# Optimization experiments

Hardware: AMD Instinct MI355X
Metric: run time of the kernel (lower is better)

The kernel has to match this reference:

```python
import jax, jax.numpy as jnp
import numpy as np


def _ln(x, g, b):
    m = x.mean(-1, keepdims=True)
    v = ((x - m) ** 2).mean(-1, keepdims=True)
    return (x - m) / jnp.sqrt(v + 1e-5) * g + b


def setup_inputs() -> dict:
    B, N, NC, EC = 4, 512, 128, 32
    KN, KE = 10, 5
    OC = 2 * EC  # NodeEdgeCombiner out_channels = 2*edge_channels
    key = jax.random.key(0)
    ks = jax.random.split(key, 16)
    s = lambda k, *sh: jax.random.normal(k, sh, jnp.float32) * 0.05
    return dict(
        node=jax.random.normal(ks[0], (B, N, NC), jnp.float32),
        edge=jax.random.normal(ks[1], (B, N, N, EC), jnp.float32),
        block_id=jnp.sort(jax.random.randint(ks[2], (B, N), 0, 16), axis=-1),
        virtual_mask=jax.random.bernoulli(ks[3], 0.1, (B, N)),
        W_nt=s(ks[4], 2 * EC + NC, NC), b_nt=jnp.zeros((NC,), jnp.float32),
        W_n1=s(ks[5], NC, 2 * OC), b_n1=jnp.zeros((2 * OC,), jnp.float32),
        W_e1=s(ks[6], EC, OC), b_e1=jnp.zeros((OC,), jnp.float32),
        W_f1=s(ks[7], OC, OC), b_f1=jnp.zeros((OC,), jnp.float32),
        W_f2=s(ks[8], OC, OC), b_f2=jnp.zeros((OC,), jnp.float32),
        W_no1=s(ks[9], NC, NC), b_no1=jnp.zeros((NC,), jnp.float32),
        g_no=jnp.ones((NC,), jnp.float32), be_no=jnp.zeros((NC,), jnp.float32),
        W_no2=s(ks[10], NC, KN), b_no2=jnp.zeros((KN,), jnp.float32),
        W_eo1=s(ks[11], OC, EC), b_eo1=jnp.zeros((EC,), jnp.float32),
        g_eo=jnp.ones((EC,), jnp.float32), be_eo=jnp.zeros((EC,), jnp.float32),
        W_eo2=s(ks[12], EC, KE), b_eo2=jnp.zeros((KE,), jnp.float32),
    )


def reference(node, edge, block_id, virtual_mask,
              W_nt, b_nt, W_n1, b_n1, W_e1, b_e1, W_f1, b_f1, W_f2, b_f2,
              W_no1, b_no1, g_no, be_no, W_no2, b_no2,
              W_eo1, b_eo1, g_eo, be_eo, W_eo2, b_eo2):
    silu = jax.nn.silu
    # masks from block ids
    nm = block_id >= 0                                   # B x N node mask
    bi = block_id[:, :, None]
    bj = block_id[:, None, :]
    pv = nm[:, :, None] & nm[:, None, :]
    # causal block mask: i may see j in strictly earlier blocks, or same block
    # unless i is a virtual (next-block placeholder) node
    causal = pv & ((bi > bj) | ((bi == bj) & ~virtual_mask[:, :, None]))
    em = causal | jnp.swapaxes(causal, 1, 2)             # symmetric edge mask
    nodem = node * nm[..., None]
    edgem = edge * em[..., None]
    # edge_to_node: masked mean of causal incoming & outgoing edges -> 2*EC
    c = causal.astype(edge.dtype)
    x_in = jnp.einsum('bijc,bij->bic', edgem, c) / jnp.maximum(c.sum(2), 1.0)[..., None]
    x_out = jnp.einsum('bjic,bji->bic', edgem, c) / jnp.maximum(c.sum(1), 1.0)[..., None]
    # node_transform: Linear + SiLU, then re-mask
    h = silu(jnp.concatenate([x_in, x_out, nodem], -1) @ W_nt + b_nt) * nm[..., None]
    # NodeEdgeCombiner (simple=False)
    e = edgem @ W_e1 + b_e1                              # B x N x N x OC
    n = h @ W_n1 + b_n1                                  # B x N x 2*OC
    n1, n2 = jnp.split(n, 2, axis=-1)
    npair = n1[:, None, :, :] + n2[:, :, None, :]        # outer-sum: n1[j]+n2[i]
    e = silu(npair + e + silu(npair @ W_f1 + b_f1) * silu(e @ W_f2 + b_f2))
    e = e + jnp.swapaxes(e, 1, 2)                        # symmetrize
    e = e * em[..., None]
    # output MLP heads (Linear -> LN -> SiLU -> Linear), masked
    node_logit = (silu(_ln(h @ W_no1 + b_no1, g_no, be_no)) @ W_no2 + b_no2) * nm[..., None]
    edge_logit = (silu(_ln(e @ W_eo1 + b_eo1, g_eo, be_eo)) @ W_eo2 + b_eo2) * em[..., None]
    return node_logit, edge_logit
```

## Files before the change

### kernel.cpp

```cpp
#include <hip/hip_runtime.h>

#define NQ 512
#define NC 128
#define EC 32
#define OC 64

__device__ __forceinline__ float silu_f(float x) {
    return x / (1.0f + __expf(-x));
}

__global__ void decode_mask_kernel(const unsigned char* __restrict__ raw,
                                   int* __restrict__ out, int n) {
    __shared__ int cntA, cntN;
    int t = threadIdx.x;
    if (t == 0) { cntA = 0; cntN = 0; }
    __syncthreads();
    int la = 0, ln = 0;
    for (int idx = t; idx < n; idx += blockDim.x) {
        unsigned char v = raw[idx];
        if (v) { if ((idx & 3) == 0) la++; else ln++; }
    }
    if (la) atomicAdd(&cntA, la);
    if (ln) atomicAdd(&cntN, ln);
    __syncthreads();
    int a = cntA, nn = cntN;
    for (int i = t; i < n; i += blockDim.x) {
        int v;
        if (a > 0 && nn == 0)      v = ((const int*)raw)[i];
        else if (a == 0)           v = (((const float*)raw)[i] != 0.0f);
        else                       v = (raw[i] != 0);
        out[i] = v;
    }
}

__global__ __launch_bounds__(128) void node_kernel(
    const float* __restrict__ node, const float* __restrict__ edge,
    const int* __restrict__ block_id, const int* __restrict__ vmd,
    const float* __restrict__ W_nt, const float* __restrict__ b_nt,
    const float* __restrict__ W_n1, const float* __restrict__ b_n1,
    const float* __restrict__ W_f1, const float* __restrict__ b_f1,
    const float* __restrict__ W_no1, const float* __restrict__ b_no1,
    const float* __restrict__ g_no, const float* __restrict__ be_no,
    const float* __restrict__ W_no2, const float* __restrict__ b_no2,
    float* __restrict__ n_ws, float* __restrict__ q1_ws, float* __restrict__ q2_ws,
    float* __restrict__ out_node) {
    const int bi = blockIdx.x;
    const int b = bi >> 9, i = bi & (NQ - 1);
    const int t = threadIdx.x;

    __shared__ int   sid[NQ];
    __shared__ int   svm[NQ];
    __shared__ float xcat[192];
    __shared__ float rin[4][32];
    __shared__ float rout[4][32];
    __shared__ int   rcin[4], rcout[4];
    __shared__ float hbuf[128];
    __shared__ float red[128];
    __shared__ float nbuf[128];
    __shared__ float zbuf[128];

    for (int k = t; k < NQ; k += 128) {
        sid[k] = block_id[b * NQ + k];
        svm[k] = vmd[b * NQ + k];
    }
    __syncthreads();

    const int  id_i = sid[i];
    const int  vm_i = svm[i];
    const bool nm_i = (id_i >= 0);

    const int c = t & 31, g = t >> 5;
    float accin = 0.f, accout = 0.f;
    int   cntin = 0, cntout = 0;
    const float* erow = edge + ((size_t)(b * NQ + i)) * NQ * EC;
    const float* ecol = edge + ((size_t)b * NQ * NQ + i) * EC;
    for (int j = g; j < NQ; j += 4) {
        int  id_j = sid[j];
        bool nm_j = (id_j >= 0);
        bool pv = nm_i && nm_j;
        bool cin  = pv && ((id_i > id_j) || (id_i == id_j && !vm_i));
        bool cout = pv && ((id_j > id_i) || (id_j == id_i && !svm[j]));
        if (cin)  { accin  += erow[j * EC + c]; cntin++; }
        if (cout) { accout += ecol[(size_t)j * NQ * EC + c]; cntout++; }
    }
    rin[g][c] = accin;
    rout[g][c] = accout;
    if (c == 0) { rcin[g] = cntin; rcout[g] = cntout; }
    __syncthreads();

    if (t < 32) {
        float s = rin[0][t] + rin[1][t] + rin[2][t] + rin[3][t];
        float cnt = (float)(rcin[0] + rcin[1] + rcin[2] + rcin[3]);
        xcat[t] = s / fmaxf(cnt, 1.0f);
    } else if (t < 64) {
        int tc = t - 32;
        float s = rout[0][tc] + rout[1][tc] + rout[2][tc] + rout[3][tc];
        float cnt = (float)(rcout[0] + rcout[1] + rcout[2] + rcout[3]);
        xcat[t] = s / fmaxf(cnt, 1.0f);
    }
    {
        float nv = node[(size_t)(b * NQ + i) * NC + t];
        xcat[64 + t] = nm_i ? nv : 0.0f;
    }
    __syncthreads();

    float acc = b_nt[t];
    #pragma unroll 4
    for (int k = 0; k < 192; ++k) acc += xcat[k] * W_nt[k * NC + t];
    float h = nm_i ? silu_f(acc) : 0.0f;
    hbuf[t] = h;
    __syncthreads();

    float accn = b_n1[t];
    float u = b_no1[t];
    #pragma unroll 4
    for (int k = 0; k < 128; ++k) {
        float hk = hbuf[k];
        accn += hk * W_n1[k * 128 + t];
        u    += hk * W_no1[k * 128 + t];
    }
    n_ws[(size_t)(b * NQ + i) * 128 + t] = accn;

    nbuf[t] = accn;
    red[t] = u;
    __syncthreads();

    {
        int cc = t & 63;
        const float* src = nbuf + ((t < 64) ? 0 : 64);
        float q = (t < 64) ? 0.0f : b_f1[cc];
        #pragma unroll 4
        for (int k = 0; k < 64; ++k) q += src[k] * W_f1[k * 64 + cc];
        float* dst = (t < 64) ? q1_ws : q2_ws;
        dst[(size_t)(b * NQ + i) * 64 + cc] = q;
    }

    for (int s = 64; s > 0; s >>= 1) { if (t < s) red[t] += red[t + s]; __syncthreads(); }
    float m = red[0] * (1.0f / 128.0f);
    __syncthreads();
    float d = u - m;
    red[t] = d * d;
    __syncthreads();
    for (int s = 64; s > 0; s >>= 1) { if (t < s) red[t] += red[t + s]; __syncthreads(); }
    float var = red[0] * (1.0f / 128.0f);
    float z = silu_f(d * rsqrtf(var + 1e-5f) * g_no[t] + be_no[t]);
    zbuf[t] = z;
    __syncthreads();

    if (t < 10) {
        float o = b_no2[t];
        #pragma unroll 4
        for (int k2 = 0; k2 < 128; ++k2) o += zbuf[k2] * W_no2[k2 * 10 + t];
        out_node[(size_t)(b * NQ + i) * 10 + t] = nm_i ? o : 0.0f;
    }
}

__global__ __launch_bounds__(256, 4) void edge_kernel(
    const float* __restrict__ edge, const int* __restrict__ block_id,
    const int* __restrict__ vmd, const float* __restrict__ n_ws,
    const float* __restrict__ q1_ws, const float* __restrict__ q2_ws,
    const float* __restrict__ W_e1, const float* __restrict__ b_e1,
    const float* __restrict__ W_f2, const float* __restrict__ b_f2,
    const float* __restrict__ W_eo1, const float* __restrict__ b_eo1,
    const float* __restrict__ g_eo, const float* __restrict__ be_eo,
    const float* __restrict__ W_eo2, const float* __restrict__ b_eo2,
    float* __restrict__ out_edge) {
    __shared__ float einT[32][64];
    __shared__ float e0T[64][64];
    __shared__ float red2[2][4][64];
    __shared__ float oBuf[4][64][5];

    const int tid = threadIdx.x;
    const int p = tid & 63;
    const int w = __builtin_amdgcn_readfirstlane(tid >> 6);
    const int bid = blockIdx.x;

    int b, ib0, jb0;
    bool tail;
    if (bid < 8192) {
        b = bid >> 11;
        int rem = bid & 2047;
        ib0 = rem >> 2;
        jb0 = ib0 + (rem & 3) * 64;
        tail = false;
    } else {
        int t2 = bid - 8192;
        b = t2 >> 2;
        ib0 = (t2 & 3) * 64;
        jb0 = 0;
        tail = true;
    }
    const int i_p = tail ? (ib0 + p) : ib0;
    const int j_p = tail ? (i_p + 256) : ((jb0 + p) & (NQ - 1));

    const float* nb0 = n_ws  + (size_t)b * NQ * 128;
    const float* q1t = q1_ws + (size_t)b * NQ * 64;
    const float* q2t = q2_ws + (size_t)b * NQ * 64;

    float es[16];
    #pragma unroll
    for (int u = 0; u < 16; ++u) es[u] = 0.0f;

    #pragma unroll 1
    for (int d = 0; d < 2; ++d) {
        {
            const int pr = tid >> 2, u = tid & 3;
            const int i_r = tail ? (ib0 + pr) : ib0;
            const int j_r = tail ? (i_r + 256) : ((jb0 + pr) & (NQ - 1));
            const size_t rowbase = d == 0
                ? (((size_t)(b * NQ) + i_r) * NQ + j_r) * EC
                : (((size_t)(b * NQ) + j_r) * NQ + i_r) * EC;
            const float4* src = (const float4*)(edge + rowbase);
            float4 v0 = src[u];
            float4 v1 = src[u + 4];
            einT[4 * u + 0][pr] = v0.x; einT[4 * u + 1][pr] = v0.y;
            einT[4 * u + 2][pr] = v0.z; einT[4 * u + 3][pr] = v0.w;
            einT[4 * (u + 4) + 0][pr] = v1.x; einT[4 * (u + 4) + 1][pr] = v1.y;
            einT[4 * (u + 4) + 2][pr] = v1.z; einT[4 * (u + 4) + 3][pr] = v1.w;
        }
        __syncthreads();

        float e0c[16];
        #pragma unroll
        for (int u = 0; u < 16; ++u) e0c[u] = b_e1[w * 16 + u];
        #pragma unroll 4
        for (int k = 0; k < EC; ++k) {
            float ek = einT[k][p];
            const float* wr = W_e1 + k * OC + w * 16;
            #pragma unroll
            for (int u = 0; u < 16; ++u) e0c[u] += ek * wr[u];
        }
        #pragma unroll
        for (int u = 0; u < 16; ++u) e0T[w * 16 + u][p] = e0c[u];
        __syncthreads();

        float t2a[16];
        #pragma unroll
        for (int u = 0; u < 16; ++u) t2a[u] = b_f2[w * 16 + u];
        #pragma unroll 4
        for (int k = 0; k < OC; ++k) {
            float e0k = e0T[k][p];
            const float* wr = W_f2 + k * OC + w * 16;
            #pragma unroll
            for (int u = 0; u < 16; ++u) t2a[u] += e0k * wr[u];
        }

        {
            const int ja = d == 0 ? j_p : i_p;
            const int ib = d == 0 ? i_p : j_p;
            const float* pq1 = q1t + (size_t)ja * 64 + w * 16;
            const float* pq2 = q2t + (size_t)ib * 64 + w * 16;
            const float* pn1 = nb0 + (size_t)ja * 128 + w * 16;
            const float* pn2 = nb0 + (size_t)ib * 128 + 64 + w * 16;
            #pragma unroll
            for (int v4 = 0; v4 < 4; ++v4) {
                float4 a1 = ((const float4*)pq1)[v4];
                float4 a2 = ((const float4*)pq2)[v4];
                float4 b1 = ((const float4*)pn1)[v4];
                float4 b2 = ((const float4*)pn2)[v4];
                float q1r[4] = {a1.x, a1.y, a1.z, a1.w};
                float q2r[4] = {a2.x, a2.y, a2.z, a2.w};
                float n1r[4] = {b1.x, b1.y, b1.z, b1.w};
                float n2r[4] = {b2.x, b2.y, b2.z, b2.w};
                #pragma unroll
                for (int r = 0; r < 4; ++r) {
                    int c = v4 * 4 + r;
                    float t1 = silu_f(q1r[r] + q2r[r]);
                    float t2 = silu_f(t2a[c]);
                    es[c] += silu_f(n1r[r] + n2r[r] + e0c[c] + t1 * t2);
                }
            }
        }
        __syncthreads();
    }

    #pragma unroll
    for (int u = 0; u < 16; ++u) e0T[w * 16 + u][p] = es[u];
    __syncthreads();

    const int c0 = w * 8;
    float y[8];
    #pragma unroll
    for (int u = 0; u < 8; ++u) y[u] = b_eo1[c0 + u];
    #pragma unroll 4
    for (int k = 0; k < OC; ++k) {
        float esk = e0T[k][p];
        const float* wr = W_eo1 + k * 32 + c0;
        #pragma unroll
        for (int u = 0; u < 8; ++u) y[u] += esk * wr[u];
    }

    float s1 = 0.f, s2 = 0.f;
    #pragma unroll
    for (int u = 0; u < 8; ++u) { s1 += y[u]; s2 += y[u] * y[u]; }
    red2[0][w][p] = s1;
    red2[1][w][p] = s2;
    __syncthreads();
    float S1 = red2[0][0][p] + red2[0][1][p] + red2[0][2][p] + red2[0][3][p];
    float S2 = red2[1][0][p] + red2[1][1][p] + red2[1][2][p] + red2[1][3][p];
    float mean = S1 * (1.0f / 32.0f);
    float var  = S2 * (1.0f / 32.0f) - mean * mean;
    float rs = rsqrtf(var + 1e-5f);

    float o[5] = {0.f, 0.f, 0.f, 0.f, 0.f};
    #pragma unroll
    for (int u = 0; u < 8; ++u) {
        float z = silu_f((y[u] - mean) * rs * g_eo[c0 + u] + be_eo[c0 + u]);
        const float* wr = W_eo2 + (c0 + u) * 5;
        #pragma unroll
        for (int q = 0; q < 5; ++q) o[q] += z * wr[q];
    }
    #pragma unroll
    for (int q = 0; q < 5; ++q) oBuf[w][p][q] = o[q];
    __syncthreads();

    if (w == 0) {
        const int id_i = block_id[b * NQ + i_p], id_j = block_id[b * NQ + j_p];
        const int vm_i = vmd[b * NQ + i_p],      vm_j = vmd[b * NQ + j_p];
        const bool em = (id_i >= 0) && (id_j >= 0) &&
                        ((id_i != id_j) || (!vm_i) || (!vm_j));
        float* oe1 = out_edge + (((size_t)(b * NQ) + i_p) * NQ + j_p) * 5;
        float* oe2 = out_edge + (((size_t)(b * NQ) + j_p) * NQ + i_p) * 5;
        #pragma unroll
        for (int q = 0; q < 5; ++q) {
            float vq = b_eo2[q] + oBuf[0][p][q] + oBuf[1][p][q]
                                + oBuf[2][p][q] + oBuf[3][p][q];
            vq = em ? vq : 0.0f;
            oe1[q] = vq;
            oe2[q] = vq;
        }
    }
}

extern "C" void kernel_launch(void* const* d_in, const int* in_sizes, int n_in,
                              void* d_out, int out_size, void* d_ws, size_t ws_size,
                              hipStream_t stream) {
    const float* node     = (const float*)d_in[0];
    const float* edge     = (const float*)d_in[1];
    const int*   block_id = (const int*)d_in[2];
    const void*  vm_raw   = d_in[3];
    const float* W_nt  = (const float*)d_in[4];
    const float* b_nt  = (const float*)d_in[5];
    const float* W_n1  = (const float*)d_in[6];
    const float* b_n1  = (const float*)d_in[7];
    const float* W_e1  = (const float*)d_in[8];
    const float* b_e1  = (const float*)d_in[9];
    const float* W_f1  = (const float*)d_in[10];
    const float* b_f1  = (const float*)d_in[11];
    const float* W_f2  = (const float*)d_in[12];
    const float* b_f2  = (const float*)d_in[13];
    const float* W_no1 = (const float*)d_in[14];
    const float* b_no1 = (const float*)d_in[15];
    const float* g_no  = (const float*)d_in[16];
    const float* be_no = (const float*)d_in[17];
    const float* W_no2 = (const float*)d_in[18];
    const float* b_no2 = (const float*)d_in[19];
    const float* W_eo1 = (const float*)d_in[20];
    const float* b_eo1 = (const float*)d_in[21];
    const float* g_eo  = (const float*)d_in[22];
    const float* be_eo = (const float*)d_in[23];
    const float* W_eo2 = (const float*)d_in[24];
    const float* b_eo2 = (const float*)d_in[25];

    char* ws = (char*)d_ws;
    int*   vmd  = (int*)ws;
    float* n_ws = (float*)(ws + 8192);
    float* q1_ws = (float*)(ws + 8192 + (1 << 20));
    float* q2_ws = (float*)(ws + 8192 + (1 << 20) + (512 << 10));
    float* out_node = (float*)d_out;
    float* out_edge = out_node + 4 * 512 * 10;

    decode_mask_kernel<<<1, 256, 0, stream>>>((const unsigned char*)vm_raw, vmd, 4 * 512);
    node_kernel<<<4 * 512, 128, 0, stream>>>(
        node, edge, block_id, vmd,
        W_nt, b_nt, W_n1, b_n1, W_f1, b_f1, W_no1, b_no1, g_no, be_no, W_no2, b_no2,
        n_ws, q1_ws, q2_ws, out_node);
    edge_kernel<<<8192 + 16, 256, 0, stream>>>(
        edge, block_id, vmd, n_ws, q1_ws, q2_ws,
        W_e1, b_e1, W_f2, b_f2,
        W_eo1, b_eo1, g_eo, be_eo, W_eo2, b_eo2, out_edge);
}
```

Before: 598.1 us.

## Split masked edge row/column sums into tiled partial-sum kernel; pad edge LDS

Moves the masked incoming/outgoing edge mean out of the per-node kernel into a separate 64x64 tile kernel. Each tile reads its edge block once, writes per-tile partial sums for both directions, and the node kernel then reduces eight partials per node. This replaces the old strided column gather (stride N*EC), which had poor coalescing. The edge kernel also overlays its LDS buffers with padding (stride 66) and raises the occupancy hint from 4 to 6 waves. The cost is an extra launch and a workspace round trip, and the tile kernel only launches 256 blocks.

```diff
diff --git a/kernel.cpp b/kernel.cpp
--- a/kernel.cpp
+++ b/kernel.cpp
@@ -33,9 +33,78 @@
     }
 }
 
-__global__ __launch_bounds__(128) void node_kernel(
-    const float* __restrict__ node, const float* __restrict__ edge,
-    const int* __restrict__ block_id, const int* __restrict__ vmd,
+__global__ __launch_bounds__(256) void tile_sum_kernel(
+    const float* __restrict__ edge, const int* __restrict__ block_id,
+    const int* __restrict__ vmd,
+    float* __restrict__ xin_part, float* __restrict__ xout_part) {
+    __shared__ float wmask[64][64];
+    __shared__ int idI[64], vmI[64], idJ[64], vmJ[64];
+
+    const int t = threadIdx.x;
+    const int bid = blockIdx.x;
+    const int b = bid >> 6, It = (bid >> 3) & 7, Jt = bid & 7;
+    const int I0 = It * 64, J0 = Jt * 64;
+
+    if (t < 64)       { idI[t] = block_id[b * NQ + I0 + t]; vmI[t] = vmd[b * NQ + I0 + t]; }
+    else if (t < 128) { int u = t - 64; idJ[u] = block_id[b * NQ + J0 + u]; vmJ[u] = vmd[b * NQ + J0 + u]; }
+    __syncthreads();
+
+    for (int idx = t; idx < 4096; idx += 256) {
+        int a = idx >> 6, bb = idx & 63;
+        int ida = idI[a], idb = idJ[bb];
+        bool w = (ida >= 0) && (idb >= 0) &&
+                 ((ida > idb) || (ida == idb && !vmI[a]));
+        wmask[a][bb] = w ? 1.0f : 0.0f;
+    }
+    __syncthreads();
+
+    const float* base = edge + (((size_t)(b * NQ) + I0) * NQ + J0) * EC;
+
+    {
+        const int bb1 = t >> 3, c0 = (t & 7) * 4;
+        float a1x = 0.f, a1y = 0.f, a1z = 0.f, a1w = 0.f;
+        float a2x = 0.f, a2y = 0.f, a2z = 0.f, a2w = 0.f;
+        for (int a = 0; a < 64; ++a) {
+            const float4* row = (const float4*)(base + (size_t)a * NQ * EC);
+            float4 v1 = row[t];
+            float4 v2 = row[t + 256];
+            float w1 = wmask[a][bb1];
+            float w2 = wmask[a][bb1 + 32];
+            a1x += w1 * v1.x; a1y += w1 * v1.y; a1z += w1 * v1.z; a1w += w1 * v1.w;
+            a2x += w2 * v2.x; a2y += w2 * v2.y; a2z += w2 * v2.z; a2w += w2 * v2.w;
+        }
+        float4 o1 = {a1x, a1y, a1z, a1w};
+        float4 o2 = {a2x, a2y, a2z, a2w};
+        *(float4*)(xout_part + ((size_t)(b * 8 + It) * NQ + J0 + bb1) * EC + c0) = o1;
+        *(float4*)(xout_part + ((size_t)(b * 8 + It) * NQ + J0 + bb1 + 32) * EC + c0) = o2;
+    }
+
+    {
+        const int c = t & 31, g = t >> 5;
+        float acc[8];
+        #pragma unroll
+        for (int k = 0; k < 8; ++k) acc[k] = 0.0f;
+        #pragma unroll 1
+        for (int k = 0; k < 8; ++k) {
+            const int a = g + 8 * k;
+            const float* rowa = base + (size_t)a * NQ * EC + c;
+            float s = 0.f;
+            #pragma unroll 4
+            for (int bb = 0; bb < 64; ++bb) s += wmask[a][bb] * rowa[bb * EC];
+            acc[k] = s;
+        }
+        #pragma unroll
+        for (int k = 0; k < 8; ++k) {
+            const int a = g + 8 * k;
+            xin_part[((size_t)(b * 8 + Jt) * NQ + I0 + a) * EC + c] = acc[k];
+        }
+    }
+}
+
+__global__ __launch_bounds__(128) void node2_kernel(
+    const float* __restrict__ node, const int* __restrict__ block_id,
+    const int* __restrict__ vmd,
+    const float* __restrict__ xin_part, const float* __restrict__ xout_part,
     const float* __restrict__ W_nt, const float* __restrict__ b_nt,
     const float* __restrict__ W_n1, const float* __restrict__ b_n1,
     const float* __restrict__ W_f1, const float* __restrict__ b_f1,
@@ -50,10 +119,8 @@
 
     __shared__ int   sid[NQ];
     __shared__ int   svm[NQ];
+    __shared__ int   redi[128], redo[128];
     __shared__ float xcat[192];
-    __shared__ float rin[4][32];
-    __shared__ float rout[4][32];
-    __shared__ int   rcin[4], rcout[4];
     __shared__ float hbuf[128];
     __shared__ float red[128];
     __shared__ float nbuf[128];
@@ -69,34 +136,37 @@
     const int  vm_i = svm[i];
     const bool nm_i = (id_i >= 0);
 
-    const int c = t & 31, g = t >> 5;
-    float accin = 0.f, accout = 0.f;
-    int   cntin = 0, cntout = 0;
-    const float* erow = edge + ((size_t)(b * NQ + i)) * NQ * EC;
-    const float* ecol = edge + ((size_t)b * NQ * NQ + i) * EC;
-    for (int j = g; j < NQ; j += 4) {
-        int  id_j = sid[j];
-        bool nm_j = (id_j >= 0);
-        bool pv = nm_i && nm_j;
-        bool cin  = pv && ((id_i > id_j) || (id_i == id_j && !vm_i));
-        bool cout = pv && ((id_j > id_i) || (id_j == id_i && !svm[j]));
-        if (cin)  { accin  += erow[j * EC + c]; cntin++; }
-        if (cout) { accout += ecol[(size_t)j * NQ * EC + c]; cntout++; }
-    }
-    rin[g][c] = accin;
-    rout[g][c] = accout;
-    if (c == 0) { rcin[g] = cntin; rcout[g] = cntout; }
-    __syncthreads();
+    int ci = 0, co = 0;
+    #pragma unroll
+    for (int r = 0; r < 4; ++r) {
+        int j = t + 128 * r;
+        int idj = sid[j];
+        bool pv = nm_i && (idj >= 0);
+        if (pv && ((id_i > idj) || (id_i == idj && !vm_i)))  ci++;
+        if (pv && ((idj > id_i) || (idj == id_i && !svm[j]))) co++;
+    }
+    redi[t] = ci; redo[t] = co;
+    __syncthreads();
+    for (int s = 64; s > 0; s >>= 1) {
+        if (t < s) { redi[t] += redi[t + s]; redo[t] += redo[t + s]; }
+        __syncthreads();
+    }
+    const float cnt_in  = fmaxf((float)redi[0], 1.0f);
+    const float cnt_out = fmaxf((float)redo[0], 1.0f);
 
     if (t < 32) {
-        float s = rin[0][t] + rin[1][t] + rin[2][t] + rin[3][t];
-        float cnt = (float)(rcin[0] + rcin[1] + rcin[2] + rcin[3]);
-        xcat[t] = s / fmaxf(cnt, 1.0f);
+        float s = 0.f;
+        #pragma unroll
+        for (int q = 0; q < 8; ++q)
+            s += xin_part[((size_t)(b * 8 + q) * NQ + i) * EC + t];
+        xcat[t] = s / cnt_in;
     } else if (t < 64) {
-        int tc = t - 32;
-        float s = rout[0][tc] + rout[1][tc] + rout[2][tc] + rout[3][tc];
-        float cnt = (float)(rcout[0] + rcout[1] + rcout[2] + rcout[3]);
-        xcat[t] = s / fmaxf(cnt, 1.0f);
+        int c = t - 32;
+        float s = 0.f;
+        #pragma unroll
+        for (int q = 0; q < 8; ++q)
+            s += xout_part[((size_t)(b * 8 + q) * NQ + i) * EC + c];
+        xcat[t] = s / cnt_out;
     }
     {
         float nv = node[(size_t)(b * NQ + i) * NC + t];
@@ -155,7 +225,7 @@
     }
 }
 
-__global__ __launch_bounds__(256, 4) void edge_kernel(
+__global__ __launch_bounds__(256, 6) void edge_kernel(
     const float* __restrict__ edge, const int* __restrict__ block_id,
     const int* __restrict__ vmd, const float* __restrict__ n_ws,
     const float* __restrict__ q1_ws, const float* __restrict__ q2_ws,
@@ -165,10 +235,10 @@
     const float* __restrict__ g_eo, const float* __restrict__ be_eo,
     const float* __restrict__ W_eo2, const float* __restrict__ b_eo2,
     float* __restrict__ out_edge) {
-    __shared__ float einT[32][64];
     __shared__ float e0T[64][64];
-    __shared__ float red2[2][4][64];
-    __shared__ float oBuf[4][64][5];
+    __shared__ float smA[32 * 66];
+    float* red2 = smA;
+    float* oBuf = smA + 512;
 
     const int tid = threadIdx.x;
     const int p = tid & 63;
@@ -213,10 +283,10 @@
             const float4* src = (const float4*)(edge + rowbase);
             float4 v0 = src[u];
             float4 v1 = src[u + 4];
-            einT[4 * u + 0][pr] = v0.x; einT[4 * u + 1][pr] = v0.y;
-            einT[4 * u + 2][pr] = v0.z; einT[4 * u + 3][pr] = v0.w;
-            einT[4 * (u + 4) + 0][pr] = v1.x; einT[4 * (u + 4) + 1][pr] = v1.y;
-            einT[4 * (u + 4) + 2][pr] = v1.z; einT[4 * (u + 4) + 3][pr] = v1.w;
+            smA[(4 * u + 0) * 66 + pr] = v0.x; smA[(4 * u + 1) * 66 + pr] = v0.y;
+            smA[(4 * u + 2) * 66 + pr] = v0.z; smA[(4 * u + 3) * 66 + pr] = v0.w;
+            smA[(4 * (u + 4) + 0) * 66 + pr] = v1.x; smA[(4 * (u + 4) + 1) * 66 + pr] = v1.y;
+            smA[(4 * (u + 4) + 2) * 66 + pr] = v1.z; smA[(4 * (u + 4) + 3) * 66 + pr] = v1.w;
         }
         __syncthreads();
 
@@ -225,7 +295,7 @@
         for (int u = 0; u < 16; ++u) e0c[u] = b_e1[w * 16 + u];
         #pragma unroll 4
         for (int k = 0; k < EC; ++k) {
-            float ek = einT[k][p];
+            float ek = smA[k * 66 + p];
             const float* wr = W_e1 + k * OC + w * 16;
             #pragma unroll
             for (int u = 0; u < 16; ++u) e0c[u] += ek * wr[u];
@@ -293,11 +363,11 @@
     float s1 = 0.f, s2 = 0.f;
     #pragma unroll
     for (int u = 0; u < 8; ++u) { s1 += y[u]; s2 += y[u] * y[u]; }
-    red2[0][w][p] = s1;
-    red2[1][w][p] = s2;
-    __syncthreads();
-    float S1 = red2[0][0][p] + red2[0][1][p] + red2[0][2][p] + red2[0][3][p];
-    float S2 = red2[1][0][p] + red2[1][1][p] + red2[1][2][p] + red2[1][3][p];
+    red2[0 * 256 + w * 64 + p] = s1;
+    red2[1 * 256 + w * 64 + p] = s2;
+    __syncthreads();
+    float S1 = red2[p] + red2[64 + p] + red2[128 + p] + red2[192 + p];
+    float S2 = red2[256 + p] + red2[320 + p] + red2[384 + p] + red2[448 + p];
     float mean = S1 * (1.0f / 32.0f);
     float var  = S2 * (1.0f / 32.0f) - mean * mean;
     float rs = rsqrtf(var + 1e-5f);
@@ -311,7 +381,7 @@
         for (int q = 0; q < 5; ++q) o[q] += z * wr[q];
     }
     #pragma unroll
-    for (int q = 0; q < 5; ++q) oBuf[w][p][q] = o[q];
+    for (int q = 0; q < 5; ++q) oBuf[(w * 64 + p) * 5 + q] = o[q];
     __syncthreads();
 
     if (w == 0) {
@@ -323,8 +393,8 @@
         float* oe2 = out_edge + (((size_t)(b * NQ) + j_p) * NQ + i_p) * 5;
         #pragma unroll
         for (int q = 0; q < 5; ++q) {
-            float vq = b_eo2[q] + oBuf[0][p][q] + oBuf[1][p][q]
-                                + oBuf[2][p][q] + oBuf[3][p][q];
+            float vq = b_eo2[q] + oBuf[(0 * 64 + p) * 5 + q] + oBuf[(1 * 64 + p) * 5 + q]
+                                + oBuf[(2 * 64 + p) * 5 + q] + oBuf[(3 * 64 + p) * 5 + q];
             vq = em ? vq : 0.0f;
             oe1[q] = vq;
             oe2[q] = vq;
@@ -363,16 +433,19 @@
     const float* b_eo2 = (const float*)d_in[25];
 
     char* ws = (char*)d_ws;
-    int*   vmd  = (int*)ws;
-    float* n_ws = (float*)(ws + 8192);
+    int*   vmd   = (int*)ws;
+    float* n_ws  = (float*)(ws + 8192);
     float* q1_ws = (float*)(ws + 8192 + (1 << 20));
     float* q2_ws = (float*)(ws + 8192 + (1 << 20) + (512 << 10));
+    float* xin_part  = (float*)(ws + 8192 + (2 << 20));
+    float* xout_part = (float*)(ws + 8192 + (4 << 20));
     float* out_node = (float*)d_out;
     float* out_edge = out_node + 4 * 512 * 10;
 
     decode_mask_kernel<<<1, 256, 0, stream>>>((const unsigned char*)vm_raw, vmd, 4 * 512);
-    node_kernel<<<4 * 512, 128, 0, stream>>>(
-        node, edge, block_id, vmd,
+    tile_sum_kernel<<<256, 256, 0, stream>>>(edge, block_id, vmd, xin_part, xout_part);
+    node2_kernel<<<4 * 512, 128, 0, stream>>>(
+        node, block_id, vmd, xin_part, xout_part,
         W_nt, b_nt, W_n1, b_n1, W_f1, b_f1, W_no1, b_no1, g_no, be_no, W_no2, b_no2,
         n_ws, q1_ws, q2_ws, out_node);
     edge_kernel<<<8192 + 16, 256, 0, stream>>>(
```

Measured after the change: 699.8 us. 17.0% more time.
